# Performance work log

Measured on AMD Instinct MI355X. Metric: run time of the kernel, lower is better.

Reference implementation:

```python
import jax, jax.numpy as jnp
import numpy as np

TINY = 1e-6  # TINY_NUMBER in the source repo
H, W, S = 256, 512, 64
N = H * W

def _unit(x, axis=-1):
    return x / jnp.maximum(jnp.linalg.norm(x, axis=axis, keepdims=True), 1e-4)

def setup_inputs() -> dict:
    key = jax.random.key(0)
    ks = jax.random.split(key, 9)
    normal = _unit(jax.random.normal(ks[0], (H, W, 3), jnp.float32))
    albedo = jax.random.uniform(ks[1], (H, W, 3), jnp.float32)
    roughness = jax.random.uniform(ks[2], (H, W, 1), jnp.float32)
    points = jax.random.normal(ks[3], (H, W, 3), jnp.float32)
    cam_position = jax.random.normal(ks[4], (3,), jnp.float32)
    light_dir_diff = _unit(jax.random.normal(ks[5], (N, S, 3), jnp.float32))
    diffuse_lighting = jax.random.uniform(ks[6], (N, S, 3), jnp.float32)
    h_dir_specular = _unit(jax.random.normal(ks[7], (N, S, 3), jnp.float32))
    specular_lighting = jax.random.uniform(ks[8], (N, S, 3), jnp.float32)
    return {"normal": normal, "albedo": albedo, "roughness": roughness,
            "points": points, "cam_position": cam_position,
            "light_dir_diff": light_dir_diff, "diffuse_lighting": diffuse_lighting,
            "h_dir_specular": h_dir_specular, "specular_lighting": specular_lighting}

def reference(normal, albedo, roughness, points, cam_position,
              light_dir_diff, diffuse_lighting, h_dir_specular, specular_lighting):
    env_h, env_w, _ = normal.shape
    n = normal.reshape(-1, 3)        # [N,3]
    a = albedo.reshape(-1, 3)        # [N,3]
    r = roughness.reshape(-1, 1)     # [N,1]
    p = points.reshape(-1, 3)        # [N,3]
    # view = F.normalize(cam - p, eps=1e-4): x / clamp(||x||, min=eps)
    d = cam_position[None, :] - p
    view = d / jnp.maximum(jnp.linalg.norm(d, axis=-1, keepdims=True), 1e-4)  # [N,3]

    def cdot(x, y):  # clamped dot over last axis, keepdim -> [...,1]
        return jnp.clip(jnp.sum(x * y, axis=-1, keepdims=True), 0.0, 1.0)

    # ---- diffuse: sum_s L * (albedo/pi) * ndl * 2*pi / S ----
    ndl_d = cdot(n[:, None, :], light_dir_diff)                      # [N,S,1]
    diffuse = jnp.sum(diffuse_lighting * (a[:, None, :] / np.pi) * ndl_d
                      * (2.0 * np.pi), axis=1) / S                   # [N,3]

    # ---- specular: GGX-style split-sum with importance-sampled half vectors ----
    v = view[:, None, :]                                             # [N,1,3]
    h = h_dir_specular                                               # [N,S,3]
    vdh = cdot(h, v)                                                 # [N,S,1]
    l_spec = 2.0 * vdh * h - v                                       # [N,S,3]
    ndl = cdot(n[:, None, :], l_spec)                                # [N,S,1]
    ndh = cdot(n[:, None, :], h)                                     # [N,S,1]
    ndv = cdot(n, view)[:, None, :]                                  # [N,1,1]
    f = 0.04 + 0.96 * jnp.exp2((-5.55472 * vdh - 6.98316) * vdh)     # Fresnel approx
    k = (r[:, None, :] + 1.0) ** 2 / 8.0                             # [N,1,1]
    g1_ndv = ndv / jnp.maximum(ndv * (1.0 - k) + k, TINY)
    g1_ndl = ndl / jnp.maximum(ndl * (1.0 - k) + k, TINY)
    brdf = f * (g1_ndl * g1_ndv) / jnp.maximum(4.0 * ndl * ndv, TINY)
    specular = jnp.sum(specular_lighting * brdf * ndl * 4.0 * vdh
                       / jnp.maximum(ndh, TINY), axis=1) / S         # [N,3]

    return (diffuse + specular).reshape(env_h, env_w, 3)
```

## Files before the change

kernel.cpp:

```cpp
#include <hip/hip_runtime.h>

#define TINY 1e-6f

constexpr int N_PIX = 256 * 512;

__device__ __forceinline__ float clamp01(float x) {
    return fminf(fmaxf(x, 0.0f), 1.0f);
}

__device__ __forceinline__ float frcp(float x) {
    return __builtin_amdgcn_rcpf(x);
}

__device__ __forceinline__ float cget(const float4& a, const float4& b, const float4& c, int i) {
    switch (i) {
        case 0:  return a.x; case 1:  return a.y; case 2:  return a.z; case 3:  return a.w;
        case 4:  return b.x; case 5:  return b.y; case 6:  return b.z; case 7:  return b.w;
        case 8:  return c.x; case 9:  return c.y; case 10: return c.z; default: return c.w;
    }
}

__global__ void __launch_bounds__(256)
shade_kernel(const float* __restrict__ normal,
             const float* __restrict__ albedo,
             const float* __restrict__ roughness,
             const float* __restrict__ points,
             const float* __restrict__ cam,
             const float* __restrict__ ldir,
             const float* __restrict__ dlight,
             const float* __restrict__ hdir,
             const float* __restrict__ slight,
             float* __restrict__ out)
{
    const int t   = threadIdx.x;
    const int grp = t >> 4;
    const int sub = t & 15;
    const int pix = blockIdx.x * 16 + grp;

    const size_t fbase = (size_t)pix * 192 + (size_t)sub * 12;
    const float4* Lp = (const float4*)(ldir   + fbase);
    const float4* Dp = (const float4*)(dlight + fbase);
    const float4* Hp = (const float4*)(hdir   + fbase);
    const float4* Sp = (const float4*)(slight + fbase);
    const float4 L0 = Lp[0], L1 = Lp[1], L2 = Lp[2];
    const float4 D0 = Dp[0], D1 = Dp[1], D2 = Dp[2];
    const float4 H0 = Hp[0], H1 = Hp[1], H2 = Hp[2];
    const float4 S0 = Sp[0], S1 = Sp[1], S2 = Sp[2];

    const float nx = normal[pix * 3 + 0];
    const float ny = normal[pix * 3 + 1];
    const float nz = normal[pix * 3 + 2];
    const float r  = roughness[pix];
    const float px = points[pix * 3 + 0];
    const float py = points[pix * 3 + 1];
    const float pz = points[pix * 3 + 2];
    const float cx = cam[0], cy = cam[1], cz = cam[2];

    const float dx = cx - px, dy = cy - py, dz = cz - pz;
    const float len = sqrtf(dx * dx + dy * dy + dz * dz);
    const float inv = frcp(fmaxf(len, 1e-4f));
    const float vx = dx * inv, vy = dy * inv, vz = dz * inv;

    const float ndv = clamp01(nx * vx + ny * vy + nz * vz);
    const float k   = (r + 1.0f) * (r + 1.0f) * 0.125f;
    const float omk = 1.0f - k;
    const float g1v = ndv * frcp(fmaxf(ndv * omk + k, TINY));

    float dacc0 = 0.f, dacc1 = 0.f, dacc2 = 0.f;
    float sacc0 = 0.f, sacc1 = 0.f, sacc2 = 0.f;

#pragma unroll
    for (int j = 0; j < 4; ++j) {
        const int e = j * 3;
        const float lx = cget(L0, L1, L2, e + 0);
        const float ly = cget(L0, L1, L2, e + 1);
        const float lz = cget(L0, L1, L2, e + 2);
        const float d0 = cget(D0, D1, D2, e + 0);
        const float d1 = cget(D0, D1, D2, e + 1);
        const float d2 = cget(D0, D1, D2, e + 2);
        const float hx = cget(H0, H1, H2, e + 0);
        const float hy = cget(H0, H1, H2, e + 1);
        const float hz = cget(H0, H1, H2, e + 2);
        const float s0 = cget(S0, S1, S2, e + 0);
        const float s1 = cget(S0, S1, S2, e + 1);
        const float s2 = cget(S0, S1, S2, e + 2);

        const float ndl_d = clamp01(nx * lx + ny * ly + nz * lz);
        dacc0 += d0 * ndl_d;
        dacc1 += d1 * ndl_d;
        dacc2 += d2 * ndl_d;

        const float vdh = clamp01(hx * vx + hy * vy + hz * vz);
        const float tv  = 2.0f * vdh;
        const float lsx = tv * hx - vx;
        const float lsy = tv * hy - vy;
        const float lsz = tv * hz - vz;
        const float ndl = clamp01(nx * lsx + ny * lsy + nz * lsz);
        const float ndh = clamp01(nx * hx + ny * hy + nz * hz);
        const float f   = 0.04f + 0.96f * exp2f((-5.55472f * vdh - 6.98316f) * vdh);
        const float g1l = ndl * frcp(fmaxf(ndl * omk + k, TINY));
        const float brdf = f * g1l * g1v * frcp(fmaxf(4.0f * ndl * ndv, TINY));
        const float w    = brdf * ndl * 4.0f * vdh * frcp(fmaxf(ndh, TINY));
        sacc0 += s0 * w;
        sacc1 += s1 * w;
        sacc2 += s2 * w;
    }

#pragma unroll
    for (int off = 1; off < 16; off <<= 1) {
        dacc0 += __shfl_xor(dacc0, off);
        dacc1 += __shfl_xor(dacc1, off);
        dacc2 += __shfl_xor(dacc2, off);
        sacc0 += __shfl_xor(sacc0, off);
        sacc1 += __shfl_xor(sacc1, off);
        sacc2 += __shfl_xor(sacc2, off);
    }

    if (sub == 0) {
        const float ax = albedo[pix * 3 + 0];
        const float ay = albedo[pix * 3 + 1];
        const float az = albedo[pix * 3 + 2];
        const float inv_s = 1.0f / 64.0f;
        out[pix * 3 + 0] = (dacc0 * ax * 2.0f + sacc0) * inv_s;
        out[pix * 3 + 1] = (dacc1 * ay * 2.0f + sacc1) * inv_s;
        out[pix * 3 + 2] = (dacc2 * az * 2.0f + sacc2) * inv_s;
    }
}

extern "C" void kernel_launch(void* const* d_in, const int* in_sizes, int n_in,
                              void* d_out, int out_size, void* d_ws, size_t ws_size,
                              hipStream_t stream) {
    const float* normal    = (const float*)d_in[0];
    const float* albedo    = (const float*)d_in[1];
    const float* roughness = (const float*)d_in[2];
    const float* points    = (const float*)d_in[3];
    const float* cam       = (const float*)d_in[4];
    const float* ldir      = (const float*)d_in[5];
    const float* dlight    = (const float*)d_in[6];
    const float* hdir      = (const float*)d_in[7];
    const float* slight    = (const float*)d_in[8];
    float* out = (float*)d_out;

    const int blocks = N_PIX / 16;
    shade_kernel<<<blocks, 256, 0, stream>>>(normal, albedo, roughness, points,
                                             cam, ldir, dlight, hdir, slight, out);
}
```

Baseline: 344.9 us.

## Use persistent blocks with register double-buffered prefetch of next pixel group

Launches a fixed 2048 blocks that each loop over several 16-pixel groups. Each iteration prefetches the next group's sample data into a second register stage while computing the current one, so memory latency overlaps with compute. Fewer, longer-lived blocks replace one-shot blocks, at the cost of roughly doubled register use for the staged loads and possibly lower occupancy on a purely bandwidth-bound streaming kernel.

```diff
diff --git a/kernel.cpp b/kernel.cpp
--- a/kernel.cpp
+++ b/kernel.cpp
@@ -2,7 +2,9 @@
 
 #define TINY 1e-6f
 
-constexpr int N_PIX = 256 * 512;
+constexpr int N_PIX  = 256 * 512;
+constexpr int BLOCKS = 2048;
+constexpr int ITERS  = N_PIX / (BLOCKS * 16);
 
 __device__ __forceinline__ float clamp01(float x) {
     return fminf(fmaxf(x, 0.0f), 1.0f);
@@ -20,6 +22,44 @@
     }
 }
 
+struct Stage {
+    float4 L0, L1, L2;
+    float4 D0, D1, D2;
+    float4 H0, H1, H2;
+    float4 S0, S1, S2;
+    float  nx, ny, nz;
+    float  px, py, pz;
+    float  r;
+    float  ax, ay, az;
+};
+
+__device__ __forceinline__ void load_stage(Stage& st, int pix, int sub,
+        const float* __restrict__ normal, const float* __restrict__ albedo,
+        const float* __restrict__ roughness, const float* __restrict__ points,
+        const float* __restrict__ ldir, const float* __restrict__ dlight,
+        const float* __restrict__ hdir, const float* __restrict__ slight)
+{
+    const size_t fb = (size_t)pix * 192 + (size_t)sub * 12;
+    const float4* Lp = (const float4*)(ldir   + fb);
+    const float4* Dp = (const float4*)(dlight + fb);
+    const float4* Hp = (const float4*)(hdir   + fb);
+    const float4* Sp = (const float4*)(slight + fb);
+    st.L0 = Lp[0]; st.L1 = Lp[1]; st.L2 = Lp[2];
+    st.D0 = Dp[0]; st.D1 = Dp[1]; st.D2 = Dp[2];
+    st.H0 = Hp[0]; st.H1 = Hp[1]; st.H2 = Hp[2];
+    st.S0 = Sp[0]; st.S1 = Sp[1]; st.S2 = Sp[2];
+    st.nx = normal[pix * 3 + 0];
+    st.ny = normal[pix * 3 + 1];
+    st.nz = normal[pix * 3 + 2];
+    st.px = points[pix * 3 + 0];
+    st.py = points[pix * 3 + 1];
+    st.pz = points[pix * 3 + 2];
+    st.r  = roughness[pix];
+    st.ax = albedo[pix * 3 + 0];
+    st.ay = albedo[pix * 3 + 1];
+    st.az = albedo[pix * 3 + 2];
+}
+
 __global__ void __launch_bounds__(256)
 shade_kernel(const float* __restrict__ normal,
              const float* __restrict__ albedo,
@@ -35,95 +75,94 @@
     const int t   = threadIdx.x;
     const int grp = t >> 4;
     const int sub = t & 15;
-    const int pix = blockIdx.x * 16 + grp;
 
-    const size_t fbase = (size_t)pix * 192 + (size_t)sub * 12;
-    const float4* Lp = (const float4*)(ldir   + fbase);
-    const float4* Dp = (const float4*)(dlight + fbase);
-    const float4* Hp = (const float4*)(hdir   + fbase);
-    const float4* Sp = (const float4*)(slight + fbase);
-    const float4 L0 = Lp[0], L1 = Lp[1], L2 = Lp[2];
-    const float4 D0 = Dp[0], D1 = Dp[1], D2 = Dp[2];
-    const float4 H0 = Hp[0], H1 = Hp[1], H2 = Hp[2];
-    const float4 S0 = Sp[0], S1 = Sp[1], S2 = Sp[2];
-
-    const float nx = normal[pix * 3 + 0];
-    const float ny = normal[pix * 3 + 1];
-    const float nz = normal[pix * 3 + 2];
-    const float r  = roughness[pix];
-    const float px = points[pix * 3 + 0];
-    const float py = points[pix * 3 + 1];
-    const float pz = points[pix * 3 + 2];
     const float cx = cam[0], cy = cam[1], cz = cam[2];
 
-    const float dx = cx - px, dy = cy - py, dz = cz - pz;
-    const float len = sqrtf(dx * dx + dy * dy + dz * dz);
-    const float inv = frcp(fmaxf(len, 1e-4f));
-    const float vx = dx * inv, vy = dy * inv, vz = dz * inv;
+    Stage A, B;
+    {
+        const int pix0 = (blockIdx.x * ITERS + 0) * 16 + grp;
+        load_stage(A, pix0, sub, normal, albedo, roughness, points,
+                   ldir, dlight, hdir, slight);
+    }
 
-    const float ndv = clamp01(nx * vx + ny * vy + nz * vz);
-    const float k   = (r + 1.0f) * (r + 1.0f) * 0.125f;
-    const float omk = 1.0f - k;
-    const float g1v = ndv * frcp(fmaxf(ndv * omk + k, TINY));
+#pragma unroll 1
+    for (int it = 0; it < ITERS; ++it) {
+        if (it + 1 < ITERS) {
+            const int pixn = (blockIdx.x * ITERS + (it + 1)) * 16 + grp;
+            load_stage(B, pixn, sub, normal, albedo, roughness, points,
+                       ldir, dlight, hdir, slight);
+        }
 
-    float dacc0 = 0.f, dacc1 = 0.f, dacc2 = 0.f;
-    float sacc0 = 0.f, sacc1 = 0.f, sacc2 = 0.f;
+        const int pix = (blockIdx.x * ITERS + it) * 16 + grp;
+
+        const float dx = cx - A.px, dy = cy - A.py, dz = cz - A.pz;
+        const float len = sqrtf(dx * dx + dy * dy + dz * dz);
+        const float inv = frcp(fmaxf(len, 1e-4f));
+        const float vx = dx * inv, vy = dy * inv, vz = dz * inv;
+
+        const float ndv = clamp01(A.nx * vx + A.ny * vy + A.nz * vz);
+        const float k   = (A.r + 1.0f) * (A.r + 1.0f) * 0.125f;
+        const float omk = 1.0f - k;
+        const float g1v = ndv * frcp(fmaxf(ndv * omk + k, TINY));
+
+        float dacc0 = 0.f, dacc1 = 0.f, dacc2 = 0.f;
+        float sacc0 = 0.f, sacc1 = 0.f, sacc2 = 0.f;
 
 #pragma unroll
-    for (int j = 0; j < 4; ++j) {
-        const int e = j * 3;
-        const float lx = cget(L0, L1, L2, e + 0);
-        const float ly = cget(L0, L1, L2, e + 1);
-        const float lz = cget(L0, L1, L2, e + 2);
-        const float d0 = cget(D0, D1, D2, e + 0);
-        const float d1 = cget(D0, D1, D2, e + 1);
-        const float d2 = cget(D0, D1, D2, e + 2);
-        const float hx = cget(H0, H1, H2, e + 0);
-        const float hy = cget(H0, H1, H2, e + 1);
-        const float hz = cget(H0, H1, H2, e + 2);
-        const float s0 = cget(S0, S1, S2, e + 0);
-        const float s1 = cget(S0, S1, S2, e + 1);
-        const float s2 = cget(S0, S1, S2, e + 2);
+        for (int j = 0; j < 4; ++j) {
+            const int e = j * 3;
+            const float lx = cget(A.L0, A.L1, A.L2, e + 0);
+            const float ly = cget(A.L0, A.L1, A.L2, e + 1);
+            const float lz = cget(A.L0, A.L1, A.L2, e + 2);
+            const float d0 = cget(A.D0, A.D1, A.D2, e + 0);
+            const float d1 = cget(A.D0, A.D1, A.D2, e + 1);
+            const float d2 = cget(A.D0, A.D1, A.D2, e + 2);
+            const float hx = cget(A.H0, A.H1, A.H2, e + 0);
+            const float hy = cget(A.H0, A.H1, A.H2, e + 1);
+            const float hz = cget(A.H0, A.H1, A.H2, e + 2);
+            const float s0 = cget(A.S0, A.S1, A.S2, e + 0);
+            const float s1 = cget(A.S0, A.S1, A.S2, e + 1);
+            const float s2 = cget(A.S0, A.S1, A.S2, e + 2);
 
-        const float ndl_d = clamp01(nx * lx + ny * ly + nz * lz);
-        dacc0 += d0 * ndl_d;
-        dacc1 += d1 * ndl_d;
-        dacc2 += d2 * ndl_d;
+            const float ndl_d = clamp01(A.nx * lx + A.ny * ly + A.nz * lz);
+            dacc0 += d0 * ndl_d;
+            dacc1 += d1 * ndl_d;
+            dacc2 += d2 * ndl_d;
 
-        const float vdh = clamp01(hx * vx + hy * vy + hz * vz);
-        const float tv  = 2.0f * vdh;
-        const float lsx = tv * hx - vx;
-        const float lsy = tv * hy - vy;
-        const float lsz = tv * hz - vz;
-        const float ndl = clamp01(nx * lsx + ny * lsy + nz * lsz);
-        const float ndh = clamp01(nx * hx + ny * hy + nz * hz);
-        const float f   = 0.04f + 0.96f * exp2f((-5.55472f * vdh - 6.98316f) * vdh);
-        const float g1l = ndl * frcp(fmaxf(ndl * omk + k, TINY));
-        const float brdf = f * g1l * g1v * frcp(fmaxf(4.0f * ndl * ndv, TINY));
-        const float w    = brdf * ndl * 4.0f * vdh * frcp(fmaxf(ndh, TINY));
-        sacc0 += s0 * w;
-        sacc1 += s1 * w;
-        sacc2 += s2 * w;
-    }
+            const float vdh = clamp01(hx * vx + hy * vy + hz * vz);
+            const float tv  = 2.0f * vdh;
+            const float lsx = tv * hx - vx;
+            const float lsy = tv * hy - vy;
+            const float lsz = tv * hz - vz;
+            const float ndl = clamp01(A.nx * lsx + A.ny * lsy + A.nz * lsz);
+            const float ndh = clamp01(A.nx * hx + A.ny * hy + A.nz * hz);
+            const float f   = 0.04f + 0.96f * exp2f((-5.55472f * vdh - 6.98316f) * vdh);
+            const float g1l = ndl * frcp(fmaxf(ndl * omk + k, TINY));
+            const float brdf = f * g1l * g1v * frcp(fmaxf(4.0f * ndl * ndv, TINY));
+            const float w    = brdf * ndl * 4.0f * vdh * frcp(fmaxf(ndh, TINY));
+            sacc0 += s0 * w;
+            sacc1 += s1 * w;
+            sacc2 += s2 * w;
+        }
 
 #pragma unroll
-    for (int off = 1; off < 16; off <<= 1) {
-        dacc0 += __shfl_xor(dacc0, off);
-        dacc1 += __shfl_xor(dacc1, off);
-        dacc2 += __shfl_xor(dacc2, off);
-        sacc0 += __shfl_xor(sacc0, off);
-        sacc1 += __shfl_xor(sacc1, off);
-        sacc2 += __shfl_xor(sacc2, off);
-    }
+        for (int off = 1; off < 16; off <<= 1) {
+            dacc0 += __shfl_xor(dacc0, off);
+            dacc1 += __shfl_xor(dacc1, off);
+            dacc2 += __shfl_xor(dacc2, off);
+            sacc0 += __shfl_xor(sacc0, off);
+            sacc1 += __shfl_xor(sacc1, off);
+            sacc2 += __shfl_xor(sacc2, off);
+        }
 
-    if (sub == 0) {
-        const float ax = albedo[pix * 3 + 0];
-        const float ay = albedo[pix * 3 + 1];
-        const float az = albedo[pix * 3 + 2];
-        const float inv_s = 1.0f / 64.0f;
-        out[pix * 3 + 0] = (dacc0 * ax * 2.0f + sacc0) * inv_s;
-        out[pix * 3 + 1] = (dacc1 * ay * 2.0f + sacc1) * inv_s;
-        out[pix * 3 + 2] = (dacc2 * az * 2.0f + sacc2) * inv_s;
+        if (sub == 0) {
+            const float inv_s = 1.0f / 64.0f;
+            out[pix * 3 + 0] = (dacc0 * A.ax * 2.0f + sacc0) * inv_s;
+            out[pix * 3 + 1] = (dacc1 * A.ay * 2.0f + sacc1) * inv_s;
+            out[pix * 3 + 2] = (dacc2 * A.az * 2.0f + sacc2) * inv_s;
+        }
+
+        A = B;
     }
 }
 
@@ -141,7 +180,6 @@
     const float* slight    = (const float*)d_in[8];
     float* out = (float*)d_out;
 
-    const int blocks = N_PIX / 16;
-    shade_kernel<<<blocks, 256, 0, stream>>>(normal, albedo, roughness, points,
+    shade_kernel<<<BLOCKS, 256, 0, stream>>>(normal, albedo, roughness, points,
                                              cam, ldir, dlight, hdir, slight, out);
 }
```

Measured after the change: 355.6 us. 1.03x slower.

## Stage per-sample input arrays into LDS via direct global-to-LDS DMA loads

Applied to the files above, without the earlier changes.

Replaces the strided per-thread float4 global loads of the four large per-sample arrays with global_load_lds DMA transfers. Each wave copies fully contiguous 1 KB chunks into shared memory, the threads wait on vmcnt and a barrier, and then read their 12-float slices from LDS. The aim is perfectly coalesced streaming of the bandwidth-bound inputs, at the cost of 48 KB of LDS per block (which limits occupancy) and an added block-wide synchronization.

```diff
diff --git a/kernel.cpp b/kernel.cpp
--- a/kernel.cpp
+++ b/kernel.cpp
@@ -3,6 +3,8 @@
 #define TINY 1e-6f
 
 constexpr int N_PIX = 256 * 512;
+
+typedef unsigned int u32;
 
 __device__ __forceinline__ float clamp01(float x) {
     return fminf(fmaxf(x, 0.0f), 1.0f);
@@ -10,6 +12,12 @@
 
 __device__ __forceinline__ float frcp(float x) {
     return __builtin_amdgcn_rcpf(x);
+}
+
+__device__ __forceinline__ void dma16(const float* g, float* l) {
+    __builtin_amdgcn_global_load_lds(
+        (const __attribute__((address_space(1))) u32*)g,
+        (__attribute__((address_space(3))) u32*)l, 16, 0, 0);
 }
 
 __device__ __forceinline__ float cget(const float4& a, const float4& b, const float4& c, int i) {
@@ -32,20 +40,32 @@
              const float* __restrict__ slight,
              float* __restrict__ out)
 {
-    const int t   = threadIdx.x;
-    const int grp = t >> 4;
-    const int sub = t & 15;
-    const int pix = blockIdx.x * 16 + grp;
+    __shared__ float lds[4 * 3072];
 
-    const size_t fbase = (size_t)pix * 192 + (size_t)sub * 12;
-    const float4* Lp = (const float4*)(ldir   + fbase);
-    const float4* Dp = (const float4*)(dlight + fbase);
-    const float4* Hp = (const float4*)(hdir   + fbase);
-    const float4* Sp = (const float4*)(slight + fbase);
-    const float4 L0 = Lp[0], L1 = Lp[1], L2 = Lp[2];
-    const float4 D0 = Dp[0], D1 = Dp[1], D2 = Dp[2];
-    const float4 H0 = Hp[0], H1 = Hp[1], H2 = Hp[2];
-    const float4 S0 = Sp[0], S1 = Sp[1], S2 = Sp[2];
+    const int t    = threadIdx.x;
+    const int w    = t >> 6;
+    const int lane = t & 63;
+    const int stage0 = blockIdx.x * 16;
+
+    {
+        const size_t gbase = (size_t)stage0 * 192;
+        const float* garr[4] = { ldir, dlight, hdir, slight };
+#pragma unroll
+        for (int a = 0; a < 4; ++a) {
+#pragma unroll
+            for (int c = 0; c < 3; ++c) {
+                const int chunk = w * 3 + c;
+                const int foff  = chunk * 256;
+                dma16(garr[a] + gbase + foff + lane * 4,
+                      &lds[a * 3072 + foff]);
+            }
+        }
+    }
+
+    const int grp = lane >> 4;
+    const int sub = lane & 15;
+    const int pin = w * 4 + grp;
+    const int pix = stage0 + pin;
 
     const float nx = normal[pix * 3 + 0];
     const float ny = normal[pix * 3 + 1];
@@ -65,6 +85,19 @@
     const float k   = (r + 1.0f) * (r + 1.0f) * 0.125f;
     const float omk = 1.0f - k;
     const float g1v = ndv * frcp(fmaxf(ndv * omk + k, TINY));
+
+    asm volatile("s_waitcnt vmcnt(0)" ::: "memory");
+    __syncthreads();
+
+    const int lbase = pin * 192 + sub * 12;
+    const float4* Lp = (const float4*)&lds[0 * 3072 + lbase];
+    const float4* Dp = (const float4*)&lds[1 * 3072 + lbase];
+    const float4* Hp = (const float4*)&lds[2 * 3072 + lbase];
+    const float4* Sp = (const float4*)&lds[3 * 3072 + lbase];
+    const float4 L0 = Lp[0], L1 = Lp[1], L2 = Lp[2];
+    const float4 D0 = Dp[0], D1 = Dp[1], D2 = Dp[2];
+    const float4 H0 = Hp[0], H1 = Hp[1], H2 = Hp[2];
+    const float4 S0 = Sp[0], S1 = Sp[1], S2 = Sp[2];
 
     float dacc0 = 0.f, dacc1 = 0.f, dacc2 = 0.f;
     float sacc0 = 0.f, sacc1 = 0.f, sacc2 = 0.f;
@@ -100,10 +133,10 @@
         const float f   = 0.04f + 0.96f * exp2f((-5.55472f * vdh - 6.98316f) * vdh);
         const float g1l = ndl * frcp(fmaxf(ndl * omk + k, TINY));
         const float brdf = f * g1l * g1v * frcp(fmaxf(4.0f * ndl * ndv, TINY));
-        const float w    = brdf * ndl * 4.0f * vdh * frcp(fmaxf(ndh, TINY));
-        sacc0 += s0 * w;
-        sacc1 += s1 * w;
-        sacc2 += s2 * w;
+        const float wgt  = brdf * ndl * 4.0f * vdh * frcp(fmaxf(ndh, TINY));
+        sacc0 += s0 * wgt;
+        sacc1 += s1 * wgt;
+        sacc2 += s2 * wgt;
     }
 
 #pragma unroll
```

Result: no change. 344.8 us (-0.1%).
